# Kernel optimization log

Hardware: AMD Instinct MI355X
Metric: run time of the kernel (lower is better)

## Reference

```python
import jax, jax.numpy as jnp
import numpy as np

D_MODEL = 256
D_INNER = 512   # expand_factor * d_model
D_STATE = 64
DT_RANK = 4     # ceil(d_model / 64)
D_CONV = 4
B = 8
L = 144


def setup_inputs() -> dict:
    key = jax.random.key(0)
    ks = jax.random.split(key, 8)
    s = lambda k, shp, sc=0.02: jax.random.normal(k, shp, jnp.float32) * sc
    x = jax.random.normal(ks[0], (B, L, D_MODEL), jnp.float32)
    lastin = jnp.zeros((B, D_INNER, D_STATE), jnp.float32)  # accepted but unused by the scan
    W_in = s(ks[1], (2 * D_INNER, D_MODEL))              # in_proj (no bias)
    conv_w = s(ks[2], (D_INNER, 1, D_CONV), 0.1)          # depthwise conv kernel [O, I/groups, K]
    conv_b = jnp.zeros((D_INNER,), jnp.float32)
    W_x = s(ks[3], (DT_RANK + 2 * D_STATE, D_INNER))      # x_proj (no bias)
    W_dt = s(ks[4], (D_INNER, DT_RANK), 0.1)
    b_dt = jnp.full((D_INNER,), -4.0, jnp.float32)        # softplus -> small dt, like mamba init
    A_log = jnp.log(jnp.tile(jnp.arange(1, D_STATE + 1, dtype=jnp.float32), (D_INNER, 1)))
    Dp = jnp.ones((D_INNER,), jnp.float32)
    W_out = s(ks[5], (D_MODEL, D_INNER))                  # out_proj (no bias)
    return dict(x=x, lastin=lastin, W_in=W_in, conv_w=conv_w, conv_b=conv_b,
                W_x=W_x, W_dt=W_dt, b_dt=b_dt, A_log=A_log, Dp=Dp, W_out=W_out)


def _forward(x, lastin, W_in, conv_w, conv_b, W_x, W_dt, b_dt, A_log, Dp, W_out):
    # in_proj and split
    xz = jnp.einsum('bld,ed->ble', x, W_in)               # [B, L, 2*d_inner]
    ix, z = jnp.split(xz, 2, axis=-1)

    # depthwise causal-ish conv1d: torch padding=2 then slice [:L] == padding (2, 1)
    ix = jnp.swapaxes(ix, 1, 2)                            # [B, d_inner, L]
    ix = jax.lax.conv_general_dilated(
        ix, conv_w, window_strides=(1,), padding=[(2, 1)],
        feature_group_count=D_INNER, dimension_numbers=('NCH', 'OIH', 'NCH'))
    ix = ix + conv_b[None, :, None]
    ix = jnp.swapaxes(ix, 1, 2)                            # [B, L, d_inner]
    ix = jax.nn.silu(ix)

    # ssm parameterization
    A = -jnp.exp(A_log)                                    # [d_inner, d_state]
    dBC = jnp.einsum('bld,ed->ble', ix, W_x)               # [B, L, dt_rank + 2*d_state]
    dt_r = dBC[..., :DT_RANK]
    Bm = dBC[..., DT_RANK:DT_RANK + D_STATE]               # [B, L, d_state]
    Cm = dBC[..., DT_RANK + D_STATE:]                      # [B, L, d_state]
    delta = jax.nn.softplus(jnp.einsum('blr,dr->bld', dt_r, W_dt) + b_dt)  # [B, L, d_inner]

    # discretization
    deltaA = jnp.exp(delta[..., None] * A)                 # [B, L, d_inner, d_state]
    BX = (delta * ix)[..., None] * Bm[:, :, None, :]       # [B, L, d_inner, d_state]

    # sequential selective scan: h_t = deltaA_t * h_{t-1} + BX_t
    def step(h, inp):
        dA_t, bx_t = inp
        h = dA_t * h + bx_t
        return h, h

    h0 = jnp.zeros((x.shape[0], D_INNER, D_STATE), x.dtype)
    _, hs = jax.lax.scan(step, h0, (jnp.moveaxis(deltaA, 1, 0), jnp.moveaxis(BX, 1, 0)))
    # hs: [L, B, d_inner, d_state]

    y = jnp.einsum('lbdn,lbn->bld', hs, jnp.moveaxis(Cm, 1, 0))  # [B, L, d_inner]
    y = y + Dp * ix

    out = jnp.einsum('bld,ed->ble', y * jax.nn.silu(z), W_out)   # [B, L, d_model]
    return out


def reference(x, lastin, W_in, conv_w, conv_b, W_x, W_dt, b_dt, A_log, Dp, W_out):
    return _forward(x, lastin, W_in, conv_w, conv_b, W_x, W_dt, b_dt, A_log, Dp, W_out)
```

## Files before the change

### kernel.cpp

```cpp
#include <hip/hip_runtime.h>

#define B_SZ 8
#define L_SEQ 144
#define NTOK 1152
#define D_MODEL 256
#define D_INNER 512
#define D_STATE 64
#define DT_RANK 4
#define NDBC 132
#define SLAB 152064

#define BM 64
#define BN 64
#define BK 16

__device__ __forceinline__ int bc_perm(const int p) {
    return (p < DT_RANK) ? p
         : (((p - DT_RANK) & 1) ? (DT_RANK + D_STATE + ((p - DT_RANK) >> 1))
                                : (DT_RANK + ((p - DT_RANK) >> 1)));
}

template<bool A_MK, bool GN, bool CONV, bool PERM>
__global__ __launch_bounds__(256) void gemm_k(const float* __restrict__ A,
                                              const float* __restrict__ Bm,
                                              float* __restrict__ C,
                                              const int N, const int lda, const int ldb,
                                              const int ldc,
                                              const float* __restrict__ cw,
                                              const float* __restrict__ cb,
                                              const int kslab, const size_t sstride) {
    __shared__ float As[BK][BM + 4];
    __shared__ float Bs[BK][BN + 4];
    const int tid = threadIdx.x;
    const int m0 = blockIdx.y * BM;
    const int n0 = blockIdx.x * BN;
    const int kbeg = blockIdx.z * kslab;
    const int kend = kbeg + kslab;
    const int ty = tid >> 4, tx = tid & 15;
    const int lrow = tid >> 2, kq = (tid & 3) * 4;
    const int kk = tid >> 4, cc = (tid & 15) * 4;
    const int brow = PERM ? bc_perm(n0 + lrow) : (n0 + lrow);
    float acc[4][4] = {};
    float4 av, bv, cw4;
    float xm2 = 0.f, xm1 = 0.f, xp4 = 0.f, cbv = 0.f;

    auto loadA = [&](const int k0) {
        if (A_MK) {
            av = *(const float4*)(A + (size_t)(m0 + lrow) * lda + k0 + kq);
        } else {
            const float* row = A + (size_t)(k0 + kk) * lda + m0 + cc;
            av = *(const float4*)row;
            if (CONV) {
                const int t = (m0 + cc) % L_SEQ;
                xm2 = (t > 0) ? row[-2] : 0.f;
                xm1 = (t > 0) ? row[-1] : 0.f;
                xp4 = (t < L_SEQ - 4) ? row[4] : 0.f;
                cw4 = *(const float4*)(cw + (k0 + kk) * 4);
                cbv = cb[k0 + kk];
            }
        }
        if (!GN || (n0 + lrow) < N)
            bv = *(const float4*)(Bm + (size_t)brow * ldb + k0 + kq);
    };

    auto storeLDS = [&]() {
        if (A_MK) {
            As[kq + 0][lrow] = av.x; As[kq + 1][lrow] = av.y;
            As[kq + 2][lrow] = av.z; As[kq + 3][lrow] = av.w;
        } else if (CONV) {
            const float in7[7] = {xm2, xm1, av.x, av.y, av.z, av.w, xp4};
            float4 o;
            float* op = &o.x;
#pragma unroll
            for (int j = 0; j < 4; ++j) {
                float s = cbv;
                s = fmaf(cw4.x, in7[j + 0], s);
                s = fmaf(cw4.y, in7[j + 1], s);
                s = fmaf(cw4.z, in7[j + 2], s);
                s = fmaf(cw4.w, in7[j + 3], s);
                op[j] = s * __builtin_amdgcn_rcpf(1.f + __expf(-s));
            }
            *(float4*)&As[kk][cc] = o;
        } else {
            *(float4*)&As[kk][cc] = av;
        }
        Bs[kq + 0][lrow] = bv.x; Bs[kq + 1][lrow] = bv.y;
        Bs[kq + 2][lrow] = bv.z; Bs[kq + 3][lrow] = bv.w;
    };

    bv = make_float4(0.f, 0.f, 0.f, 0.f);
    loadA(kbeg);
    for (int k0 = kbeg; k0 < kend; k0 += BK) {
        __syncthreads();
        storeLDS();
        __syncthreads();
        if (k0 + BK < kend) loadA(k0 + BK);
#pragma unroll
        for (int k = 0; k < BK; ++k) {
            const float4 a4 = *(const float4*)&As[k][ty * 4];
            const float4 b4 = *(const float4*)&Bs[k][tx * 4];
            const float a_[4] = {a4.x, a4.y, a4.z, a4.w};
            const float b_[4] = {b4.x, b4.y, b4.z, b4.w};
#pragma unroll
            for (int i = 0; i < 4; ++i)
#pragma unroll
                for (int j = 0; j < 4; ++j)
                    acc[i][j] = fmaf(a_[i], b_[j], acc[i][j]);
        }
    }
    C += (size_t)blockIdx.z * sstride;
#pragma unroll
    for (int i = 0; i < 4; ++i) {
        const int gm = m0 + ty * 4 + i;
        const int gn = n0 + tx * 4;
        if (!GN || gn < N)
            *(float4*)(C + (size_t)gm * ldc + gn) =
                make_float4(acc[i][0], acc[i][1], acc[i][2], acc[i][3]);
    }
}

__global__ __launch_bounds__(256) void reduce4_k(const float4* __restrict__ in,
                                                 float4* __restrict__ out,
                                                 const int n4, const int s4) {
    const int i = blockIdx.x * 256 + threadIdx.x;
    if (i >= n4) return;
    const float4 a = in[i], b = in[i + s4], c = in[i + 2 * s4], d = in[i + 3 * s4];
    out[i] = make_float4(a.x + b.x + c.x + d.x, a.y + b.y + c.y + d.y,
                         a.z + b.z + c.z + d.z, a.w + b.w + c.w + d.w);
}

__device__ __forceinline__ float bcast(const float v, const int i) {
    return __int_as_float(__builtin_amdgcn_readlane(__float_as_int(v), i));
}

template<int CNT>
__device__ __forceinline__ void scan_chunk(const float* __restrict__ dBC,
                                           const float* __restrict__ xzT,
                                           float* __restrict__ gT,
                                           float (*__restrict__ Pw)[65],
                                           const int d, const int base, const int t0,
                                           const float An2, const float4 wdt,
                                           const float bdt, const float dpv,
                                           const float4 cw4, const float cbv,
                                           const int lane, float& h) {
    float delta_r = 0.f, dix_r = 0.f, dpix_r = 0.f, sz_r = 0.f;
    if (lane < CNT) {
        const int t = t0 + lane;
        const int tok = base + t;
        const float* row = xzT + (size_t)d * NTOK + tok;
        float s0 = cbv;
        if (t >= 2) s0 = fmaf(cw4.x, row[-2], s0);
        if (t >= 1) s0 = fmaf(cw4.y, row[-1], s0);
        s0 = fmaf(cw4.z, row[0], s0);
        if (t < L_SEQ - 1) s0 = fmaf(cw4.w, row[1], s0);
        const float ixv = s0 * __builtin_amdgcn_rcpf(1.f + __expf(-s0));

        const float4 dt4 = *(const float4*)(dBC + (size_t)tok * NDBC);
        float s = fmaf(dt4.x, wdt.x, bdt);
        s = fmaf(dt4.y, wdt.y, s);
        s = fmaf(dt4.z, wdt.z, s);
        s = fmaf(dt4.w, wdt.w, s);
        const float delta = fmaxf(s, 0.f) + __logf(1.f + __expf(-fabsf(s)));
        const float zv = xzT[(size_t)(D_INNER + d) * NTOK + tok];
        delta_r = delta;
        dix_r   = delta * ixv;
        dpix_r  = dpv * ixv;
        sz_r    = zv * __builtin_amdgcn_rcpf(1.f + __expf(-zv));
    }
#pragma unroll
    for (int i = 0; i < CNT; ++i) {
        const float2 bc = *(const float2*)(dBC + (size_t)(base + t0 + i) * NDBC
                                           + DT_RANK + 2 * lane);
        const float dlt = bcast(delta_r, i);
        const float dxv = bcast(dix_r, i);
        const float dA = __builtin_amdgcn_exp2f(dlt * An2);
        h = fmaf(dA, h, dxv * bc.x);
        Pw[i][lane] = h * bc.y;
    }
    const int tl = lane & 31, hf = lane >> 5;
    float s2 = 0.f;
    if (tl < CNT) {
#pragma unroll
        for (int j = 0; j < 32; ++j) s2 += Pw[tl][hf * 32 + j];
    }
    s2 += __shfl_xor(s2, 32, 64);
    if (hf == 0 && tl < CNT) {
        gT[(size_t)d * NTOK + base + t0 + tl] = (s2 + dpix_r) * sz_r;
    }
}

__global__ __launch_bounds__(256) void scan_k(const float* __restrict__ dBC,
                                              const float* __restrict__ xzT,
                                              const float* __restrict__ W_dt,
                                              const float* __restrict__ b_dt,
                                              const float* __restrict__ A_log,
                                              const float* __restrict__ Dp,
                                              const float* __restrict__ conv_w,
                                              const float* __restrict__ conv_b,
                                              float* __restrict__ gT) {
    __shared__ float P[4][32][65];
    const int w = threadIdx.x >> 6, lane = threadIdx.x & 63;
    const int b = blockIdx.x >> 7, dg = blockIdx.x & 127;
    const int d = (dg << 2) | w;
    const int base = b * L_SEQ;
    const float An2 = -__expf(A_log[(d << 6) + lane]) * 1.44269504088896f;
    const float4 wdt = *(const float4*)(W_dt + (d << 2));
    const float bdt = b_dt[d], dpv = Dp[d];
    const float4 cw4 = *(const float4*)(conv_w + (d << 2));
    const float cbv = conv_b[d];
    float h = 0.f;
    scan_chunk<32>(dBC, xzT, gT, P[w], d, base, 0,   An2, wdt, bdt, dpv, cw4, cbv, lane, h);
    scan_chunk<32>(dBC, xzT, gT, P[w], d, base, 32,  An2, wdt, bdt, dpv, cw4, cbv, lane, h);
    scan_chunk<32>(dBC, xzT, gT, P[w], d, base, 64,  An2, wdt, bdt, dpv, cw4, cbv, lane, h);
    scan_chunk<32>(dBC, xzT, gT, P[w], d, base, 96,  An2, wdt, bdt, dpv, cw4, cbv, lane, h);
    scan_chunk<16>(dBC, xzT, gT, P[w], d, base, 128, An2, wdt, bdt, dpv, cw4, cbv, lane, h);
}

extern "C" void kernel_launch(void* const* d_in, const int* in_sizes, int n_in,
                              void* d_out, int out_size, void* d_ws, size_t ws_size,
                              hipStream_t stream) {
    const float* x      = (const float*)d_in[0];
    const float* W_in   = (const float*)d_in[2];
    const float* conv_w = (const float*)d_in[3];
    const float* conv_b = (const float*)d_in[4];
    const float* W_x    = (const float*)d_in[5];
    const float* W_dt   = (const float*)d_in[6];
    const float* b_dt   = (const float*)d_in[7];
    const float* A_log  = (const float*)d_in[8];
    const float* Dp     = (const float*)d_in[9];
    const float* W_out  = (const float*)d_in[10];
    float* out = (float*)d_out;

    float* ws  = (float*)d_ws;
    float* xzT = ws;
    float* dBC = xzT + 1179648;
    float* gT  = dBC + 152064;
    float* sl3 = gT + 589824;
    float* sl6 = xzT;

    gemm_k<true, false, false, false><<<dim3(18, 16, 1), 256, 0, stream>>>(
        W_in, x, xzT, NTOK, D_MODEL, D_MODEL, NTOK, nullptr, nullptr, D_MODEL, 0);
    gemm_k<false, true, true, true><<<dim3(3, 18, 4), 256, 0, stream>>>(
        xzT, W_x, sl3, NDBC, NTOK, D_INNER, NDBC, conv_w, conv_b, 128, (size_t)SLAB);
    reduce4_k<<<dim3(149), 256, 0, stream>>>((const float4*)sl3, (float4*)dBC,
                                             NTOK * NDBC / 4, NTOK * NDBC / 4);
    scan_k<<<dim3(B_SZ * 128), 256, 0, stream>>>(dBC, xzT, W_dt, b_dt, A_log, Dp,
                                                 conv_w, conv_b, gT);
    gemm_k<false, false, false, false><<<dim3(4, 18, 4), 256, 0, stream>>>(
        gT, W_out, sl6, D_MODEL, NTOK, D_INNER, D_MODEL, nullptr, nullptr, 128,
        (size_t)NTOK * D_MODEL);
    reduce4_k<<<dim3(288), 256, 0, stream>>>((const float4*)sl6, (float4*)out,
                                             NTOK * D_MODEL / 4, NTOK * D_MODEL / 4);
}
```

Baseline: 141.6 us.

## Fuse split-K reductions into scan and replace out-proj split-K GEMM with direct GEMM

```diff
diff --git a/kernel.cpp b/kernel.cpp
--- a/kernel.cpp
+++ b/kernel.cpp
@@ -13,6 +13,9 @@
 #define BM 64
 #define BN 64
 #define BK 16
+
+#define CH 16
+#define NCH 9
 
 __device__ __forceinline__ int bc_perm(const int p) {
     return (p < DT_RANK) ? p
@@ -119,77 +122,57 @@
     }
 }
 
-__global__ __launch_bounds__(256) void reduce4_k(const float4* __restrict__ in,
-                                                 float4* __restrict__ out,
-                                                 const int n4, const int s4) {
-    const int i = blockIdx.x * 256 + threadIdx.x;
-    if (i >= n4) return;
-    const float4 a = in[i], b = in[i + s4], c = in[i + 2 * s4], d = in[i + 3 * s4];
-    out[i] = make_float4(a.x + b.x + c.x + d.x, a.y + b.y + c.y + d.y,
-                         a.z + b.z + c.z + d.z, a.w + b.w + c.w + d.w);
+#define BM3 32
+#define BN3 32
+#define BK3 32
+__global__ __launch_bounds__(256) void gemm3_k(const float* __restrict__ A,
+                                               const float* __restrict__ Bw,
+                                               float* __restrict__ C) {
+    __shared__ float As[BK3][BM3 + 4];
+    __shared__ float Bs[BK3][BN3 + 4];
+    const int tid = threadIdx.x;
+    const int m0 = blockIdx.y * BM3;
+    const int n0 = blockIdx.x * BN3;
+    const int ak = tid >> 3, am = (tid & 7) << 2;
+    const int bn = tid >> 3, bk = (tid & 7) << 2;
+    const int ty = tid >> 4, tx = tid & 15;
+    float acc[2][2] = {};
+    float4 av, bv;
+
+    auto load = [&](const int k0) {
+        av = *(const float4*)(A + (size_t)(k0 + ak) * NTOK + m0 + am);
+        bv = *(const float4*)(Bw + (size_t)(n0 + bn) * D_INNER + k0 + bk);
+    };
+
+    load(0);
+    for (int k0 = 0; k0 < D_INNER; k0 += BK3) {
+        __syncthreads();
+        *(float4*)&As[ak][am] = av;
+        Bs[bk + 0][bn] = bv.x; Bs[bk + 1][bn] = bv.y;
+        Bs[bk + 2][bn] = bv.z; Bs[bk + 3][bn] = bv.w;
+        __syncthreads();
+        if (k0 + BK3 < D_INNER) load(k0 + BK3);
+#pragma unroll
+        for (int k = 0; k < BK3; ++k) {
+            const float2 a2 = *(const float2*)&As[k][ty * 2];
+            const float2 b2 = *(const float2*)&Bs[k][tx * 2];
+            acc[0][0] = fmaf(a2.x, b2.x, acc[0][0]);
+            acc[0][1] = fmaf(a2.x, b2.y, acc[0][1]);
+            acc[1][0] = fmaf(a2.y, b2.x, acc[1][0]);
+            acc[1][1] = fmaf(a2.y, b2.y, acc[1][1]);
+        }
+    }
+#pragma unroll
+    for (int i = 0; i < 2; ++i)
+        *(float2*)(C + (size_t)(m0 + ty * 2 + i) * D_MODEL + n0 + tx * 2) =
+            make_float2(acc[i][0], acc[i][1]);
 }
 
 __device__ __forceinline__ float bcast(const float v, const int i) {
     return __int_as_float(__builtin_amdgcn_readlane(__float_as_int(v), i));
 }
 
-template<int CNT>
-__device__ __forceinline__ void scan_chunk(const float* __restrict__ dBC,
-                                           const float* __restrict__ xzT,
-                                           float* __restrict__ gT,
-                                           float (*__restrict__ Pw)[65],
-                                           const int d, const int base, const int t0,
-                                           const float An2, const float4 wdt,
-                                           const float bdt, const float dpv,
-                                           const float4 cw4, const float cbv,
-                                           const int lane, float& h) {
-    float delta_r = 0.f, dix_r = 0.f, dpix_r = 0.f, sz_r = 0.f;
-    if (lane < CNT) {
-        const int t = t0 + lane;
-        const int tok = base + t;
-        const float* row = xzT + (size_t)d * NTOK + tok;
-        float s0 = cbv;
-        if (t >= 2) s0 = fmaf(cw4.x, row[-2], s0);
-        if (t >= 1) s0 = fmaf(cw4.y, row[-1], s0);
-        s0 = fmaf(cw4.z, row[0], s0);
-        if (t < L_SEQ - 1) s0 = fmaf(cw4.w, row[1], s0);
-        const float ixv = s0 * __builtin_amdgcn_rcpf(1.f + __expf(-s0));
-
-        const float4 dt4 = *(const float4*)(dBC + (size_t)tok * NDBC);
-        float s = fmaf(dt4.x, wdt.x, bdt);
-        s = fmaf(dt4.y, wdt.y, s);
-        s = fmaf(dt4.z, wdt.z, s);
-        s = fmaf(dt4.w, wdt.w, s);
-        const float delta = fmaxf(s, 0.f) + __logf(1.f + __expf(-fabsf(s)));
-        const float zv = xzT[(size_t)(D_INNER + d) * NTOK + tok];
-        delta_r = delta;
-        dix_r   = delta * ixv;
-        dpix_r  = dpv * ixv;
-        sz_r    = zv * __builtin_amdgcn_rcpf(1.f + __expf(-zv));
-    }
-#pragma unroll
-    for (int i = 0; i < CNT; ++i) {
-        const float2 bc = *(const float2*)(dBC + (size_t)(base + t0 + i) * NDBC
-                                           + DT_RANK + 2 * lane);
-        const float dlt = bcast(delta_r, i);
-        const float dxv = bcast(dix_r, i);
-        const float dA = __builtin_amdgcn_exp2f(dlt * An2);
-        h = fmaf(dA, h, dxv * bc.x);
-        Pw[i][lane] = h * bc.y;
-    }
-    const int tl = lane & 31, hf = lane >> 5;
-    float s2 = 0.f;
-    if (tl < CNT) {
-#pragma unroll
-        for (int j = 0; j < 32; ++j) s2 += Pw[tl][hf * 32 + j];
-    }
-    s2 += __shfl_xor(s2, 32, 64);
-    if (hf == 0 && tl < CNT) {
-        gT[(size_t)d * NTOK + base + t0 + tl] = (s2 + dpix_r) * sz_r;
-    }
-}
-
-__global__ __launch_bounds__(256) void scan_k(const float* __restrict__ dBC,
+__global__ __launch_bounds__(512) void scan_k(const float* __restrict__ sl3,
                                               const float* __restrict__ xzT,
                                               const float* __restrict__ W_dt,
                                               const float* __restrict__ b_dt,
@@ -198,22 +181,80 @@
                                               const float* __restrict__ conv_w,
                                               const float* __restrict__ conv_b,
                                               float* __restrict__ gT) {
-    __shared__ float P[4][32][65];
-    const int w = threadIdx.x >> 6, lane = threadIdx.x & 63;
-    const int b = blockIdx.x >> 7, dg = blockIdx.x & 127;
-    const int d = (dg << 2) | w;
+    __shared__ float bc[CH][128];
+    __shared__ float P[8][CH][65];
+    const int tid = threadIdx.x;
+    const int w = tid >> 6, lane = tid & 63;
+    const int b = blockIdx.x >> 6, dg = blockIdx.x & 63;
+    const int d = (dg << 3) | w;
     const int base = b * L_SEQ;
     const float An2 = -__expf(A_log[(d << 6) + lane]) * 1.44269504088896f;
     const float4 wdt = *(const float4*)(W_dt + (d << 2));
     const float bdt = b_dt[d], dpv = Dp[d];
     const float4 cw4 = *(const float4*)(conv_w + (d << 2));
     const float cbv = conv_b[d];
+    const int srow = tid >> 5, scol = (tid & 31) << 2;
     float h = 0.f;
-    scan_chunk<32>(dBC, xzT, gT, P[w], d, base, 0,   An2, wdt, bdt, dpv, cw4, cbv, lane, h);
-    scan_chunk<32>(dBC, xzT, gT, P[w], d, base, 32,  An2, wdt, bdt, dpv, cw4, cbv, lane, h);
-    scan_chunk<32>(dBC, xzT, gT, P[w], d, base, 64,  An2, wdt, bdt, dpv, cw4, cbv, lane, h);
-    scan_chunk<32>(dBC, xzT, gT, P[w], d, base, 96,  An2, wdt, bdt, dpv, cw4, cbv, lane, h);
-    scan_chunk<16>(dBC, xzT, gT, P[w], d, base, 128, An2, wdt, bdt, dpv, cw4, cbv, lane, h);
+
+    for (int c = 0; c < NCH; ++c) {
+        const int t0 = c * CH;
+        __syncthreads();
+        {
+            const float* q = sl3 + (size_t)(base + t0 + srow) * NDBC + DT_RANK + scol;
+            const float4 q0 = *(const float4*)(q);
+            const float4 q1 = *(const float4*)(q + SLAB);
+            const float4 q2 = *(const float4*)(q + 2 * SLAB);
+            const float4 q3 = *(const float4*)(q + 3 * SLAB);
+            *(float4*)&bc[srow][scol] =
+                make_float4(q0.x + q1.x + q2.x + q3.x, q0.y + q1.y + q2.y + q3.y,
+                            q0.z + q1.z + q2.z + q3.z, q0.w + q1.w + q2.w + q3.w);
+        }
+        float delta_r = 0.f, dix_r = 0.f, dpix_r = 0.f, sz_r = 0.f;
+        if (lane < CH) {
+            const int t = t0 + lane;
+            const int tok = base + t;
+            const float* row = xzT + (size_t)d * NTOK + tok;
+            float s0 = cbv;
+            if (t >= 2) s0 = fmaf(cw4.x, row[-2], s0);
+            if (t >= 1) s0 = fmaf(cw4.y, row[-1], s0);
+            s0 = fmaf(cw4.z, row[0], s0);
+            if (t < L_SEQ - 1) s0 = fmaf(cw4.w, row[1], s0);
+            const float ixv = s0 * __builtin_amdgcn_rcpf(1.f + __expf(-s0));
+            const float* qd = sl3 + (size_t)tok * NDBC;
+            const float4 e0 = *(const float4*)(qd);
+            const float4 e1 = *(const float4*)(qd + SLAB);
+            const float4 e2 = *(const float4*)(qd + 2 * SLAB);
+            const float4 e3 = *(const float4*)(qd + 3 * SLAB);
+            float s = fmaf(e0.x + e1.x + e2.x + e3.x, wdt.x, bdt);
+            s = fmaf(e0.y + e1.y + e2.y + e3.y, wdt.y, s);
+            s = fmaf(e0.z + e1.z + e2.z + e3.z, wdt.z, s);
+            s = fmaf(e0.w + e1.w + e2.w + e3.w, wdt.w, s);
+            const float delta = fmaxf(s, 0.f) + __logf(1.f + __expf(-fabsf(s)));
+            const float zv = xzT[(size_t)(D_INNER + d) * NTOK + tok];
+            delta_r = delta;
+            dix_r   = delta * ixv;
+            dpix_r  = dpv * ixv;
+            sz_r    = zv * __builtin_amdgcn_rcpf(1.f + __expf(-zv));
+        }
+        __syncthreads();
+#pragma unroll
+        for (int i = 0; i < CH; ++i) {
+            const float2 bcv = *(const float2*)&bc[i][lane << 1];
+            const float dlt = bcast(delta_r, i);
+            const float dxv = bcast(dix_r, i);
+            const float dA = __builtin_amdgcn_exp2f(dlt * An2);
+            h = fmaf(dA, h, dxv * bcv.x);
+            P[w][i][lane] = h * bcv.y;
+        }
+        const int tl = lane & 15, qq = lane >> 4;
+        float s2 = 0.f;
+#pragma unroll
+        for (int j = 0; j < 16; ++j) s2 += P[w][tl][(qq << 4) + j];
+        s2 += __shfl_xor(s2, 16, 64);
+        s2 += __shfl_xor(s2, 32, 64);
+        if (lane < CH)
+            gT[(size_t)d * NTOK + base + t0 + lane] = (s2 + dpix_r) * sz_r;
+    }
 }
 
 extern "C" void kernel_launch(void* const* d_in, const int* in_sizes, int n_in,
@@ -233,22 +274,14 @@
 
     float* ws  = (float*)d_ws;
     float* xzT = ws;
-    float* dBC = xzT + 1179648;
-    float* gT  = dBC + 152064;
-    float* sl3 = gT + 589824;
-    float* sl6 = xzT;
+    float* sl3 = xzT + 1179648;
+    float* gT  = sl3 + 4 * SLAB;
 
     gemm_k<true, false, false, false><<<dim3(18, 16, 1), 256, 0, stream>>>(
         W_in, x, xzT, NTOK, D_MODEL, D_MODEL, NTOK, nullptr, nullptr, D_MODEL, 0);
     gemm_k<false, true, true, true><<<dim3(3, 18, 4), 256, 0, stream>>>(
         xzT, W_x, sl3, NDBC, NTOK, D_INNER, NDBC, conv_w, conv_b, 128, (size_t)SLAB);
-    reduce4_k<<<dim3(149), 256, 0, stream>>>((const float4*)sl3, (float4*)dBC,
-                                             NTOK * NDBC / 4, NTOK * NDBC / 4);
-    scan_k<<<dim3(B_SZ * 128), 256, 0, stream>>>(dBC, xzT, W_dt, b_dt, A_log, Dp,
-                                                 conv_w, conv_b, gT);
-    gemm_k<false, false, false, false><<<dim3(4, 18, 4), 256, 0, stream>>>(
-        gT, W_out, sl6, D_MODEL, NTOK, D_INNER, D_MODEL, nullptr, nullptr, 128,
-        (size_t)NTOK * D_MODEL);
-    reduce4_k<<<dim3(288), 256, 0, stream>>>((const float4*)sl6, (float4*)out,
-                                             NTOK * D_MODEL / 4, NTOK * D_MODEL / 4);
-}
+    scan_k<<<dim3(B_SZ * 64), 512, 0, stream>>>(sl3, xzT, W_dt, b_dt, A_log, Dp,
+                                                conv_w, conv_b, gT);
+    gemm3_k<<<dim3(8, 36), 256, 0, stream>>>(gT, W_out, out);
+}
```

New measurement: 148.7 us. 1.05x slower.

## Split-K the in-projection into two slabs and double split-K for later GEMMs

Applied to the files above, without the earlier changes.

```diff
diff --git a/kernel.cpp b/kernel.cpp
--- a/kernel.cpp
+++ b/kernel.cpp
@@ -9,6 +9,7 @@
 #define DT_RANK 4
 #define NDBC 132
 #define SLAB 152064
+#define XZSLAB 1179648
 
 #define BM 64
 #define BN 64
@@ -20,7 +21,7 @@
                                 : (DT_RANK + ((p - DT_RANK) >> 1)));
 }
 
-template<bool A_MK, bool GN, bool CONV, bool PERM>
+template<bool A_MK, bool GN, bool CONV, bool PERM, bool A2S>
 __global__ __launch_bounds__(256) void gemm_k(const float* __restrict__ A,
                                               const float* __restrict__ Bm,
                                               float* __restrict__ C,
@@ -28,7 +29,8 @@
                                               const int ldc,
                                               const float* __restrict__ cw,
                                               const float* __restrict__ cb,
-                                              const int kslab, const size_t sstride) {
+                                              const int kslab, const size_t sstride,
+                                              const size_t a2off) {
     __shared__ float As[BK][BM + 4];
     __shared__ float Bs[BK][BN + 4];
     const int tid = threadIdx.x;
@@ -50,11 +52,19 @@
         } else {
             const float* row = A + (size_t)(k0 + kk) * lda + m0 + cc;
             av = *(const float4*)row;
+            if (A2S) {
+                const float4 a2 = *(const float4*)(row + a2off);
+                av.x += a2.x; av.y += a2.y; av.z += a2.z; av.w += a2.w;
+            }
             if (CONV) {
                 const int t = (m0 + cc) % L_SEQ;
                 xm2 = (t > 0) ? row[-2] : 0.f;
                 xm1 = (t > 0) ? row[-1] : 0.f;
                 xp4 = (t < L_SEQ - 4) ? row[4] : 0.f;
+                if (A2S) {
+                    if (t > 0) { xm2 += row[a2off - 2]; xm1 += row[a2off - 1]; }
+                    if (t < L_SEQ - 4) xp4 += row[a2off + 4];
+                }
                 cw4 = *(const float4*)(cw + (k0 + kk) * 4);
                 cbv = cb[k0 + kk];
             }
@@ -119,14 +129,18 @@
     }
 }
 
-__global__ __launch_bounds__(256) void reduce4_k(const float4* __restrict__ in,
+__global__ __launch_bounds__(256) void reduce8_k(const float4* __restrict__ in,
                                                  float4* __restrict__ out,
                                                  const int n4, const int s4) {
     const int i = blockIdx.x * 256 + threadIdx.x;
     if (i >= n4) return;
-    const float4 a = in[i], b = in[i + s4], c = in[i + 2 * s4], d = in[i + 3 * s4];
-    out[i] = make_float4(a.x + b.x + c.x + d.x, a.y + b.y + c.y + d.y,
-                         a.z + b.z + c.z + d.z, a.w + b.w + c.w + d.w);
+    float4 a = in[i];
+#pragma unroll
+    for (int s = 1; s < 8; ++s) {
+        const float4 b = in[i + s * s4];
+        a.x += b.x; a.y += b.y; a.z += b.z; a.w += b.w;
+    }
+    out[i] = a;
 }
 
 __device__ __forceinline__ float bcast(const float v, const int i) {
@@ -135,7 +149,7 @@
 
 template<int CNT>
 __device__ __forceinline__ void scan_chunk(const float* __restrict__ dBC,
-                                           const float* __restrict__ xzT,
+                                           const float* __restrict__ xz,
                                            float* __restrict__ gT,
                                            float (*__restrict__ Pw)[65],
                                            const int d, const int base, const int t0,
@@ -147,12 +161,12 @@
     if (lane < CNT) {
         const int t = t0 + lane;
         const int tok = base + t;
-        const float* row = xzT + (size_t)d * NTOK + tok;
+        const float* row = xz + (size_t)d * NTOK + tok;
         float s0 = cbv;
-        if (t >= 2) s0 = fmaf(cw4.x, row[-2], s0);
-        if (t >= 1) s0 = fmaf(cw4.y, row[-1], s0);
-        s0 = fmaf(cw4.z, row[0], s0);
-        if (t < L_SEQ - 1) s0 = fmaf(cw4.w, row[1], s0);
+        if (t >= 2) s0 = fmaf(cw4.x, row[-2] + row[XZSLAB - 2], s0);
+        if (t >= 1) s0 = fmaf(cw4.y, row[-1] + row[XZSLAB - 1], s0);
+        s0 = fmaf(cw4.z, row[0] + row[XZSLAB], s0);
+        if (t < L_SEQ - 1) s0 = fmaf(cw4.w, row[1] + row[XZSLAB + 1], s0);
         const float ixv = s0 * __builtin_amdgcn_rcpf(1.f + __expf(-s0));
 
         const float4 dt4 = *(const float4*)(dBC + (size_t)tok * NDBC);
@@ -161,7 +175,8 @@
         s = fmaf(dt4.z, wdt.z, s);
         s = fmaf(dt4.w, wdt.w, s);
         const float delta = fmaxf(s, 0.f) + __logf(1.f + __expf(-fabsf(s)));
-        const float zv = xzT[(size_t)(D_INNER + d) * NTOK + tok];
+        const float* zp = xz + (size_t)(D_INNER + d) * NTOK + tok;
+        const float zv = zp[0] + zp[XZSLAB];
         delta_r = delta;
         dix_r   = delta * ixv;
         dpix_r  = dpv * ixv;
@@ -190,7 +205,7 @@
 }
 
 __global__ __launch_bounds__(256) void scan_k(const float* __restrict__ dBC,
-                                              const float* __restrict__ xzT,
+                                              const float* __restrict__ xz,
                                               const float* __restrict__ W_dt,
                                               const float* __restrict__ b_dt,
                                               const float* __restrict__ A_log,
@@ -209,11 +224,11 @@
     const float4 cw4 = *(const float4*)(conv_w + (d << 2));
     const float cbv = conv_b[d];
     float h = 0.f;
-    scan_chunk<32>(dBC, xzT, gT, P[w], d, base, 0,   An2, wdt, bdt, dpv, cw4, cbv, lane, h);
-    scan_chunk<32>(dBC, xzT, gT, P[w], d, base, 32,  An2, wdt, bdt, dpv, cw4, cbv, lane, h);
-    scan_chunk<32>(dBC, xzT, gT, P[w], d, base, 64,  An2, wdt, bdt, dpv, cw4, cbv, lane, h);
-    scan_chunk<32>(dBC, xzT, gT, P[w], d, base, 96,  An2, wdt, bdt, dpv, cw4, cbv, lane, h);
-    scan_chunk<16>(dBC, xzT, gT, P[w], d, base, 128, An2, wdt, bdt, dpv, cw4, cbv, lane, h);
+    scan_chunk<32>(dBC, xz, gT, P[w], d, base, 0,   An2, wdt, bdt, dpv, cw4, cbv, lane, h);
+    scan_chunk<32>(dBC, xz, gT, P[w], d, base, 32,  An2, wdt, bdt, dpv, cw4, cbv, lane, h);
+    scan_chunk<32>(dBC, xz, gT, P[w], d, base, 64,  An2, wdt, bdt, dpv, cw4, cbv, lane, h);
+    scan_chunk<32>(dBC, xz, gT, P[w], d, base, 96,  An2, wdt, bdt, dpv, cw4, cbv, lane, h);
+    scan_chunk<16>(dBC, xz, gT, P[w], d, base, 128, An2, wdt, bdt, dpv, cw4, cbv, lane, h);
 }
 
 extern "C" void kernel_launch(void* const* d_in, const int* in_sizes, int n_in,
@@ -232,23 +247,25 @@
     float* out = (float*)d_out;
 
     float* ws  = (float*)d_ws;
-    float* xzT = ws;
-    float* dBC = xzT + 1179648;
+    float* xz  = ws;
+    float* dBC = xz + 2 * XZSLAB;
     float* gT  = dBC + 152064;
     float* sl3 = gT + 589824;
-    float* sl6 = xzT;
-
-    gemm_k<true, false, false, false><<<dim3(18, 16, 1), 256, 0, stream>>>(
-        W_in, x, xzT, NTOK, D_MODEL, D_MODEL, NTOK, nullptr, nullptr, D_MODEL, 0);
-    gemm_k<false, true, true, true><<<dim3(3, 18, 4), 256, 0, stream>>>(
-        xzT, W_x, sl3, NDBC, NTOK, D_INNER, NDBC, conv_w, conv_b, 128, (size_t)SLAB);
-    reduce4_k<<<dim3(149), 256, 0, stream>>>((const float4*)sl3, (float4*)dBC,
+    float* sl6 = ws;
+
+    gemm_k<true, false, false, false, false><<<dim3(18, 16, 2), 256, 0, stream>>>(
+        W_in, x, xz, NTOK, D_MODEL, D_MODEL, NTOK, nullptr, nullptr, 128,
+        (size_t)XZSLAB, 0);
+    gemm_k<false, true, true, true, true><<<dim3(3, 18, 8), 256, 0, stream>>>(
+        xz, W_x, sl3, NDBC, NTOK, D_INNER, NDBC, conv_w, conv_b, 64, (size_t)SLAB,
+        (size_t)XZSLAB);
+    reduce8_k<<<dim3(149), 256, 0, stream>>>((const float4*)sl3, (float4*)dBC,
                                              NTOK * NDBC / 4, NTOK * NDBC / 4);
-    scan_k<<<dim3(B_SZ * 128), 256, 0, stream>>>(dBC, xzT, W_dt, b_dt, A_log, Dp,
+    scan_k<<<dim3(B_SZ * 128), 256, 0, stream>>>(dBC, xz, W_dt, b_dt, A_log, Dp,
                                                  conv_w, conv_b, gT);
-    gemm_k<false, false, false, false><<<dim3(4, 18, 4), 256, 0, stream>>>(
-        gT, W_out, sl6, D_MODEL, NTOK, D_INNER, D_MODEL, nullptr, nullptr, 128,
-        (size_t)NTOK * D_MODEL);
-    reduce4_k<<<dim3(288), 256, 0, stream>>>((const float4*)sl6, (float4*)out,
+    gemm_k<false, false, false, false, false><<<dim3(4, 18, 8), 256, 0, stream>>>(
+        gT, W_out, sl6, D_MODEL, NTOK, D_INNER, D_MODEL, nullptr, nullptr, 64,
+        (size_t)NTOK * D_MODEL, 0);
+    reduce8_k<<<dim3(288), 256, 0, stream>>>((const float4*)sl6, (float4*)out,
                                              NTOK * D_MODEL / 4, NTOK * D_MODEL / 4);
 }
```

Measured after the change: 139.4 us. Within noise of the previous version (-1.5%).
